# Performance work log

Hardware: AMD Instinct MI355X
Metric: run time of the kernel (lower is better)

Reference implementation:

```python
import jax, jax.numpy as jnp
import numpy as np

B, T, ENC_IN, DEC_IN, U = 32768, 7, 60, 36, 356


def setup_inputs() -> dict:
    key = jax.random.key(0)
    ks = jax.random.split(key, 12)
    s = 0.05  # small weight scale for numerical sanity
    return {
        "x_batch": jax.random.normal(ks[0], (B, T, ENC_IN), jnp.float32),
        "m_batch": jax.random.normal(ks[1], (B, T, DEC_IN), jnp.float32),
        "enc_kernel": jax.random.normal(ks[2], (ENC_IN, 4 * U), jnp.float32) * s,
        "enc_rec_kernel": jax.random.normal(ks[3], (U, 4 * U), jnp.float32) * s,
        "enc_bias": jnp.zeros((4 * U,), jnp.float32),
        "dec_kernel": jax.random.normal(ks[4], (DEC_IN, 4 * U), jnp.float32) * s,
        "dec_rec_kernel": jax.random.normal(ks[5], (U, 4 * U), jnp.float32) * s,
        "dec_bias": jnp.zeros((4 * U,), jnp.float32),
        "W_map": jax.random.normal(ks[6], (T * U, 768), jnp.float32) * s,
        "b_map": jnp.zeros((768,), jnp.float32),
        "W_deep1": jax.random.normal(ks[7], (768, 768), jnp.float32) * s,
        "b_deep1": jnp.zeros((768,), jnp.float32),
        "W_deep2": jax.random.normal(ks[8], (768, 768), jnp.float32) * s,
        "b_deep2": jnp.zeros((768,), jnp.float32),
        "W_out": jax.random.normal(ks[9], (768, 168), jnp.float32) * s,
        "b_out": jnp.zeros((168,), jnp.float32),
    }


def _lstm(x, K, R, b, h0, c0):
    """Keras-style LSTM. x: [B,T,D]. Returns (hs [B,T,U], h_T, c_T).
    Gate order i, f, g(candidate), o; sigmoid recurrent activation, tanh activation."""
    xz = jnp.einsum('btd,dg->btg', x, K) + b  # precompute input projections [B,T,4U]

    def step(carry, xz_t):
        h, c = carry
        z = xz_t + h @ R
        i, f, g, o = jnp.split(z, 4, axis=-1)
        c = jax.nn.sigmoid(f) * c + jax.nn.sigmoid(i) * jnp.tanh(g)
        h = jax.nn.sigmoid(o) * jnp.tanh(c)
        return (h, c), h

    (h, c), hs = jax.lax.scan(step, (h0, c0), jnp.swapaxes(xz, 0, 1))
    return jnp.swapaxes(hs, 0, 1), h, c


def reference(x_batch, m_batch, enc_kernel, enc_rec_kernel, enc_bias,
              dec_kernel, dec_rec_kernel, dec_bias,
              W_map, b_map, W_deep1, b_deep1, W_deep2, b_deep2, W_out, b_out):
    b = x_batch.shape[0]
    z = jnp.zeros((b, U), x_batch.dtype)
    # encoder: only final states used
    _, s_h, s_c = _lstm(x_batch, enc_kernel, enc_rec_kernel, enc_bias, z, z)
    # decoder: full sequence, initialized with encoder states
    decoded, _, _ = _lstm(m_batch, dec_kernel, dec_rec_kernel, dec_bias, s_h, s_c)
    f = decoded.reshape(b, -1)  # [B, 7*356]
    m = jax.nn.relu(f @ W_map + b_map)
    d = jnp.tanh(m @ W_deep1 + b_deep1)
    d = jnp.tanh(d @ W_deep2 + b_deep2)
    return d @ W_out + b_out
```

## Files before the change

### kernel.cpp

```cpp
#include <hip/hip_runtime.h>

typedef unsigned short u16;
typedef __attribute__((ext_vector_type(8))) short short8;
typedef __attribute__((ext_vector_type(4))) float f32x4;

#define B_ROWS 32768
#define T_STEPS 7
#define ENC_INd 60
#define DEC_INd 36
#define UNITS 356
#define KP_LSTM 448
#define H_OFF 64
#define HID 768
#define OUTN 168
#define OUTNP 256
#define KMAP 2688
#define HALF_E 44040192ull
#define WLSTM_E 688128

__device__ __forceinline__ u16 f2b(float f) {
  unsigned u = __builtin_bit_cast(unsigned, f);
  u += 0x7fffu + ((u >> 16) & 1u);
  return (u16)(u >> 16);
}
__device__ __forceinline__ float sigm(float x) { return 1.0f / (1.0f + __expf(-x)); }
__device__ __forceinline__ float tanhfast(float x) { return 2.0f / (1.0f + __expf(-2.0f * x)) - 1.0f; }

__global__ void fill_sentinel(float* __restrict__ out, int n, float v) {
  int i = blockIdx.x * 256 + threadIdx.x;
  int stride = gridDim.x * 256;
  for (; i < n; i += stride) out[i] = v;
}

__global__ void prep_lstm_w(const float* __restrict__ Km, const float* __restrict__ Rm,
                            const float* __restrict__ bias, int in_dim,
                            u16* __restrict__ WT, float* __restrict__ bias_r)
{
  int idx = blockIdx.x * 256 + threadIdx.x;
  if (idx >= WLSTM_E) return;
  int e    = idx & 7;
  int lane = (idx >> 3) & 63;
  int nf   = (idx >> 9) & 3;
  int t1   = idx >> 11;
  int kk   = t1 % 14;
  int g    = t1 / 14;
  int u = g * 16 + (lane & 15);
  int k = kk * 32 + ((lane >> 4) << 3) + e;
  float v = 0.f;
  if (u < UNITS) {
    int oc = nf * UNITS + u;
    if (k < in_dim) v = Km[(size_t)k * 1424 + oc];
    else if (k >= H_OFF && k < H_OFF + UNITS) v = Rm[(size_t)(k - H_OFF) * 1424 + oc];
    if (k == 0) bias_r[(u << 2) + nf] = bias[oc];
  } else if (k == 0) bias_r[(u << 2) + nf] = 0.f;
  WT[idx] = f2b(v);
}

__global__ void prep_map_w(const float* __restrict__ W, u16* __restrict__ WT)
{
  int idx = blockIdx.x * 256 + threadIdx.x;
  if (idx >= HID * KMAP) return;
  int n = idx / KMAP, k = idx - n * KMAP;
  int t = k / 384, kk = k - t * 384;
  float v = (kk < UNITS) ? W[(size_t)(t * UNITS + kk) * HID + n] : 0.f;
  WT[idx] = f2b(v);
}

__global__ void prep_mlp_w(const float* __restrict__ W, int korig, int norig, int kp,
                           u16* __restrict__ WT, int total)
{
  int idx = blockIdx.x * 256 + threadIdx.x;
  if (idx >= total) return;
  int n = idx / kp, k = idx - n * kp;
  float v = (k < korig && n < norig) ? W[(size_t)k * norig + n] : 0.f;
  WT[idx] = f2b(v);
}

__global__ __launch_bounds__(512)
void lstm_persistent(const float* __restrict__ xg, const float* __restrict__ mg,
                     const u16* __restrict__ WTe, const float* __restrict__ bre,
                     const u16* __restrict__ WTd, const float* __restrict__ brd,
                     u16* __restrict__ fbuf)
{
  __shared__ __align__(16) u16 A[2][32][KP_LSTM];

  const int tid = threadIdx.x;
  const int ns = tid >> 6;
  const int lane = tid & 63;
  const int l15 = lane & 15, l4 = lane >> 4;
  const int row0 = blockIdx.x * 32;

  float c_reg[3][2][4];
#pragma unroll
  for (int a = 0; a < 3; ++a)
#pragma unroll
    for (int b = 0; b < 2; ++b)
      c_reg[a][b][0] = c_reg[a][b][1] = c_reg[a][b][2] = c_reg[a][b][3] = 0.f;

  {
    short8 z = {};
    for (int q = tid; q < 2 * 32 * 48; q += 512) {
      int buf = q / 1536, rem = q - buf * 1536;
      int row = rem / 48, blk = 8 + (rem - row * 48);
      *(short8*)&A[buf][row][blk << 3] = z;
    }
  }

#pragma unroll 1
  for (int s = 0; s < 14; ++s) {
    const u16*  wt = (s < 7) ? WTe : WTd;
    const float* br = (s < 7) ? bre : brd;
    const float* src = (s < 7) ? xg : mg;
    const int in_dim = (s < 7) ? ENC_INd : DEC_INd;
    const int t = (s < 7) ? s : s - 7;
    const int par = s & 1;

    if (tid < 256) {
      const int row = tid >> 3, cb = tid & 7;
      const float* sp = src + ((size_t)(row0 + row) * T_STEPS + t) * in_dim;
      const int cbs = cb ^ (row & 7);
      short8 vv;
#pragma unroll
      for (int j = 0; j < 8; ++j) {
        const int cc = (cb << 3) + j;
        float v = (cc < in_dim) ? sp[cc] : 0.f;
        vv[j] = (short)f2b(v);
      }
      *(short8*)&A[par][row][cbs << 3] = vv;
    }
    __syncthreads();

#pragma unroll 1
    for (int p = 0; p < 3; ++p) {
      const int g = p * 8 + ns;
      f32x4 acc[2][4] = {};
      const u16* bp = wt + ((size_t)g * 14) * 2048 + (lane << 3);

#pragma unroll 2
      for (int kk = 0; kk < 14; ++kk) {
        short8 af[2], bf[4];
#pragma unroll
        for (int mf = 0; mf < 2; ++mf) {
          const int ra = (mf << 4) + l15;
          const int cbA = (kk << 2) + l4;
          const int cbs = (cbA & 56) | ((cbA ^ ra) & 7);
          af[mf] = *(const short8*)&A[par][ra][cbs << 3];
        }
#pragma unroll
        for (int nf = 0; nf < 4; ++nf)
          bf[nf] = *(const short8*)(bp + kk * 2048 + (nf << 9));
#pragma unroll
        for (int mf = 0; mf < 2; ++mf)
#pragma unroll
          for (int nf = 0; nf < 4; ++nf)
            acc[mf][nf] = __builtin_amdgcn_mfma_f32_16x16x32_bf16(af[mf], bf[nf], acc[mf][nf], 0, 0, 0);
      }

      const int u = (g << 4) + l15;
      const int ch = H_OFF + u, cbh = ch >> 3, cih = ch & 7;
      float bz[4];
#pragma unroll
      for (int nf = 0; nf < 4; ++nf) bz[nf] = br[(u << 2) + nf];
#pragma unroll
      for (int mf = 0; mf < 2; ++mf)
#pragma unroll
        for (int r = 0; r < 4; ++r) {
          const int row = (mf << 4) + (l4 << 2) + r;
          float zi = acc[mf][0][r] + bz[0];
          float zf = acc[mf][1][r] + bz[1];
          float zg = acc[mf][2][r] + bz[2];
          float zo = acc[mf][3][r] + bz[3];
          float ig = sigm(zi), fg = sigm(zf);
          float gg = tanhfast(zg), og = sigm(zo);
          float cn = fg * c_reg[p][mf][r] + ig * gg;
          c_reg[p][mf][r] = cn;
          float hv = og * tanhfast(cn);
          u16 hb = f2b(hv);
          const int cbs = (cbh & 56) | ((cbh ^ row) & 7);
          A[par ^ 1][row][(cbs << 3) + cih] = hb;
          if (s >= 7) {
            const int grow = row0 + row;
            fbuf[(size_t)(grow >> 14) * HALF_E
                 + ((size_t)(grow & 16383) * T_STEPS + t) * 384 + u] = hb;
          }
        }
    }
  }
}

template<int MODE>
__global__ __launch_bounds__(256)
void mlp_gemm(const u16* __restrict__ A, int lda, int kp,
              const u16* __restrict__ WT, const float* __restrict__ bias, int nreal,
              u16* __restrict__ outb, float* __restrict__ outf, int ldo)
{
  __shared__ __align__(16) u16 lds_a[128 * 64];
  __shared__ __align__(16) u16 lds_b[128 * 64];
  const int tid = threadIdx.x;
  const int wid = tid >> 6, lane = tid & 63;
  const int wm = (wid >> 1) << 6, wn = (wid & 1) << 6;
  const int l15 = lane & 15, l4 = lane >> 4;
  const int r0 = tid >> 3, c8 = tid & 7;
  const size_t abase = (size_t)blockIdx.x * 128 * lda;
  const size_t bbase = (size_t)blockIdx.y * 128 * kp;

  f32x4 acc[4][4] = {};

  for (int kt = 0; kt < kp; kt += 64) {
#pragma unroll
    for (int p = 0; p < 4; ++p) {
      int r = r0 + p * 32;
      short8 va = *(const short8*)(A + abase + (size_t)r * lda + kt + (c8 << 3));
      *(short8*)&lds_a[(r << 6) + ((c8 ^ (r & 7)) << 3)] = va;
      short8 vb = *(const short8*)(WT + bbase + (size_t)r * kp + kt + (c8 << 3));
      *(short8*)&lds_b[(r << 6) + ((c8 ^ (r & 7)) << 3)] = vb;
    }
    __syncthreads();
#pragma unroll
    for (int kk = 0; kk < 2; ++kk) {
      short8 af[4], bfr[4];
#pragma unroll
      for (int mf = 0; mf < 4; ++mf) {
        int ra = wm + (mf << 4) + l15;
        int cb = (kk << 2) + l4;
        af[mf] = *(const short8*)&lds_a[(ra << 6) + ((cb ^ (ra & 7)) << 3)];
      }
#pragma unroll
      for (int nf = 0; nf < 4; ++nf) {
        int rb = wn + (nf << 4) + l15;
        int cb = (kk << 2) + l4;
        bfr[nf] = *(const short8*)&lds_b[(rb << 6) + ((cb ^ (rb & 7)) << 3)];
      }
#pragma unroll
      for (int mf = 0; mf < 4; ++mf)
#pragma unroll
        for (int nf = 0; nf < 4; ++nf)
          acc[mf][nf] = __builtin_amdgcn_mfma_f32_16x16x32_bf16(af[mf], bfr[nf], acc[mf][nf], 0, 0, 0);
    }
    __syncthreads();
  }

#pragma unroll
  for (int mf = 0; mf < 4; ++mf) {
    int rowb = blockIdx.x * 128 + wm + (mf << 4) + (l4 << 2);
#pragma unroll
    for (int r = 0; r < 4; ++r) {
      int row = rowb + r;
#pragma unroll
      for (int nf = 0; nf < 4; ++nf) {
        int n = blockIdx.y * 128 + wn + (nf << 4) + l15;
        float v = acc[mf][nf][r];
        size_t oi = (size_t)row * ldo + n;
        if (MODE == 3) {
          outb[oi] = f2b(tanhfast(v + bias[n]));
        } else if (MODE == 5) {
          outb[oi] = f2b(fmaxf(v + bias[n], 0.f));
        } else {
          if (n < nreal) outf[oi] = v + bias[n];
        }
      }
    }
  }
}

extern "C" void kernel_launch(void* const* d_in, const int* in_sizes, int n_in,
                              void* d_out, int out_size, void* d_ws, size_t ws_size,
                              hipStream_t stream)
{
  const float* x    = (const float*)d_in[0];
  const float* m    = (const float*)d_in[1];
  const float* ek   = (const float*)d_in[2];
  const float* erk  = (const float*)d_in[3];
  const float* eb   = (const float*)d_in[4];
  const float* dk   = (const float*)d_in[5];
  const float* drk  = (const float*)d_in[6];
  const float* dbi  = (const float*)d_in[7];
  const float* wmap = (const float*)d_in[8];
  const float* bmap = (const float*)d_in[9];
  const float* wd1  = (const float*)d_in[10];
  const float* bd1  = (const float*)d_in[11];
  const float* wd2  = (const float*)d_in[12];
  const float* bd2  = (const float*)d_in[13];
  const float* wout = (const float*)d_in[14];
  const float* bout = (const float*)d_in[15];

  char* ws = (char*)d_ws;
  size_t off = 0;
  auto alloc = [&](size_t bytes) { char* p = ws + off; off += (bytes + 255) & ~(size_t)255; return p; };

  u16*   WT_enc  = (u16*)  alloc((size_t)WLSTM_E * 2);
  u16*   WT_dec  = (u16*)  alloc((size_t)WLSTM_E * 2);
  float* b_enc_r = (float*)alloc((size_t)384 * 4 * 4);
  float* b_dec_r = (float*)alloc((size_t)384 * 4 * 4);
  u16*   WT_map  = (u16*)  alloc((size_t)HID * KMAP * 2);
  u16*   WT_d1   = (u16*)  alloc((size_t)HID * HID * 2);
  u16*   WT_d2   = (u16*)  alloc((size_t)HID * HID * 2);
  u16*   WT_out  = (u16*)  alloc((size_t)OUTNP * HID * 2);
  u16*   m1_h1   = (u16*)  alloc((size_t)16384 * HID * 2);
  u16*   fbuf    = (u16*)  alloc((size_t)2 * HALF_E * 2);
  const size_t NEED = off;

  if (ws_size < NEED) {
    fill_sentinel<<<256, 256, 0, stream>>>((float*)d_out, out_size, (float)(ws_size >> 20));
    return;
  }

  u16* fb_h0 = fbuf;
  u16* fb_h1 = fbuf + HALF_E;
  u16* m1_h0 = fb_h1;
  u16* m2_h0 = fb_h0;
  u16* m2_h1 = fb_h0 + (size_t)16384 * HID;
  u16* m3_h0 = fb_h1;
  u16* m3_h1 = m1_h1;

  prep_lstm_w<<<(WLSTM_E + 255) / 256, 256, 0, stream>>>(ek, erk, eb, ENC_INd, WT_enc, b_enc_r);
  prep_lstm_w<<<(WLSTM_E + 255) / 256, 256, 0, stream>>>(dk, drk, dbi, DEC_INd, WT_dec, b_dec_r);
  prep_map_w<<<((HID * KMAP) + 255) / 256, 256, 0, stream>>>(wmap, WT_map);
  prep_mlp_w<<<((HID * HID) + 255) / 256, 256, 0, stream>>>(wd1, HID, HID, HID, WT_d1, HID * HID);
  prep_mlp_w<<<((HID * HID) + 255) / 256, 256, 0, stream>>>(wd2, HID, HID, HID, WT_d2, HID * HID);
  prep_mlp_w<<<((OUTNP * HID) + 255) / 256, 256, 0, stream>>>(wout, HID, OUTN, HID, WT_out, OUTNP * HID);

  lstm_persistent<<<1024, 512, 0, stream>>>(x, m, WT_enc, b_enc_r, WT_dec, b_dec_r, fbuf);

  mlp_gemm<5><<<dim3(128, 6), 256, 0, stream>>>(fb_h1, KMAP, KMAP, WT_map, bmap, HID, m1_h1, nullptr, HID);
  mlp_gemm<5><<<dim3(128, 6), 256, 0, stream>>>(fb_h0, KMAP, KMAP, WT_map, bmap, HID, m1_h0, nullptr, HID);
  mlp_gemm<3><<<dim3(128, 6), 256, 0, stream>>>(m1_h0, HID, HID, WT_d1, bd1, HID, m2_h0, nullptr, HID);
  mlp_gemm<3><<<dim3(128, 6), 256, 0, stream>>>(m1_h1, HID, HID, WT_d1, bd1, HID, m2_h1, nullptr, HID);
  mlp_gemm<3><<<dim3(128, 6), 256, 0, stream>>>(m2_h0, HID, HID, WT_d2, bd2, HID, m3_h0, nullptr, HID);
  mlp_gemm<3><<<dim3(128, 6), 256, 0, stream>>>(m2_h1, HID, HID, WT_d2, bd2, HID, m3_h1, nullptr, HID);
  mlp_gemm<4><<<dim3(128, 2), 256, 0, stream>>>(m3_h0, HID, HID, WT_out, bout, OUTN,
                                                nullptr, (float*)d_out, OUTN);
  mlp_gemm<4><<<dim3(128, 2), 256, 0, stream>>>(m3_h1, HID, HID, WT_out, bout, OUTN,
                                                nullptr, (float*)d_out + (size_t)16384 * OUTN, OUTN);
}
```

Before: 1.460 ms.

## Double LSTM rows per block and spill cell state to scratch global memory

The persistent LSTM kernel now handles 64 batch rows per block (512 blocks) instead of 32, so each weight fragment loaded from global memory feeds twice as many MFMAs. Doubling the accumulators would push register pressure too high, so the cell state no longer lives in registers. It is written to and read back from global scratch each step, reusing the output buffer, an m1 buffer and a new workspace slice. This cuts weight traffic and instruction overhead in exchange for extra global memory traffic for cell state, a larger LDS footprint and possibly lower occupancy.

```diff
diff --git a/kernel.cpp b/kernel.cpp
--- a/kernel.cpp
+++ b/kernel.cpp
@@ -17,6 +17,7 @@
 #define KMAP 2688
 #define HALF_E 44040192ull
 #define WLSTM_E 688128
+#define CG_BLK 6144
 
 __device__ __forceinline__ u16 f2b(float f) {
   unsigned u = __builtin_bit_cast(unsigned, f);
@@ -80,29 +81,29 @@
 void lstm_persistent(const float* __restrict__ xg, const float* __restrict__ mg,
                      const u16* __restrict__ WTe, const float* __restrict__ bre,
                      const u16* __restrict__ WTd, const float* __restrict__ brd,
-                     u16* __restrict__ fbuf)
-{
-  __shared__ __align__(16) u16 A[2][32][KP_LSTM];
+                     u16* __restrict__ fbuf,
+                     f32x4* __restrict__ cg0, f32x4* __restrict__ cg1, f32x4* __restrict__ cg2)
+{
+  __shared__ __align__(16) u16 A[2][64][KP_LSTM];
 
   const int tid = threadIdx.x;
   const int ns = tid >> 6;
   const int lane = tid & 63;
   const int l15 = lane & 15, l4 = lane >> 4;
-  const int row0 = blockIdx.x * 32;
-
-  float c_reg[3][2][4];
-#pragma unroll
-  for (int a = 0; a < 3; ++a)
-#pragma unroll
-    for (int b = 0; b < 2; ++b)
-      c_reg[a][b][0] = c_reg[a][b][1] = c_reg[a][b][2] = c_reg[a][b][3] = 0.f;
+  const int blk = blockIdx.x;
+  const int row0 = blk * 64;
+
+  f32x4* cgb;
+  if (blk < 224)      cgb = cg0 + (size_t)blk * CG_BLK;
+  else if (blk < 480) cgb = cg1 + (size_t)(blk - 224) * CG_BLK;
+  else                cgb = cg2 + (size_t)(blk - 480) * CG_BLK;
 
   {
     short8 z = {};
-    for (int q = tid; q < 2 * 32 * 48; q += 512) {
-      int buf = q / 1536, rem = q - buf * 1536;
-      int row = rem / 48, blk = 8 + (rem - row * 48);
-      *(short8*)&A[buf][row][blk << 3] = z;
+    for (int q = tid; q < 6144; q += 512) {
+      int buf = q / 3072, rem = q - buf * 3072;
+      int row = rem / 48, blkc = 8 + (rem - row * 48);
+      *(short8*)&A[buf][row][blkc << 3] = z;
     }
   }
 
@@ -115,7 +116,7 @@
     const int t = (s < 7) ? s : s - 7;
     const int par = s & 1;
 
-    if (tid < 256) {
+    {
       const int row = tid >> 3, cb = tid & 7;
       const float* sp = src + ((size_t)(row0 + row) * T_STEPS + t) * in_dim;
       const int cbs = cb ^ (row & 7);
@@ -133,27 +134,44 @@
 #pragma unroll 1
     for (int p = 0; p < 3; ++p) {
       const int g = p * 8 + ns;
-      f32x4 acc[2][4] = {};
+      f32x4 acc[4][4] = {};
       const u16* bp = wt + ((size_t)g * 14) * 2048 + (lane << 3);
 
-#pragma unroll 2
+#pragma unroll 1
       for (int kk = 0; kk < 14; ++kk) {
-        short8 af[2], bf[4];
-#pragma unroll
-        for (int mf = 0; mf < 2; ++mf) {
-          const int ra = (mf << 4) + l15;
-          const int cbA = (kk << 2) + l4;
-          const int cbs = (cbA & 56) | ((cbA ^ ra) & 7);
-          af[mf] = *(const short8*)&A[par][ra][cbs << 3];
-        }
+        short8 bf[4];
 #pragma unroll
         for (int nf = 0; nf < 4; ++nf)
           bf[nf] = *(const short8*)(bp + kk * 2048 + (nf << 9));
-#pragma unroll
-        for (int mf = 0; mf < 2; ++mf)
-#pragma unroll
-          for (int nf = 0; nf < 4; ++nf)
-            acc[mf][nf] = __builtin_amdgcn_mfma_f32_16x16x32_bf16(af[mf], bf[nf], acc[mf][nf], 0, 0, 0);
+        const int cbA = (kk << 2) + l4;
+        {
+          short8 af0[2];
+#pragma unroll
+          for (int mf = 0; mf < 2; ++mf) {
+            const int ra = (mf << 4) + l15;
+            const int cbs = (cbA & 56) | ((cbA ^ ra) & 7);
+            af0[mf] = *(const short8*)&A[par][ra][cbs << 3];
+          }
+#pragma unroll
+          for (int mf = 0; mf < 2; ++mf)
+#pragma unroll
+            for (int nf = 0; nf < 4; ++nf)
+              acc[mf][nf] = __builtin_amdgcn_mfma_f32_16x16x32_bf16(af0[mf], bf[nf], acc[mf][nf], 0, 0, 0);
+        }
+        {
+          short8 af1[2];
+#pragma unroll
+          for (int mf = 0; mf < 2; ++mf) {
+            const int ra = ((mf + 2) << 4) + l15;
+            const int cbs = (cbA & 56) | ((cbA ^ ra) & 7);
+            af1[mf] = *(const short8*)&A[par][ra][cbs << 3];
+          }
+#pragma unroll
+          for (int mf = 0; mf < 2; ++mf)
+#pragma unroll
+            for (int nf = 0; nf < 4; ++nf)
+              acc[mf + 2][nf] = __builtin_amdgcn_mfma_f32_16x16x32_bf16(af1[mf], bf[nf], acc[mf + 2][nf], 0, 0, 0);
+        }
       }
 
       const int u = (g << 4) + l15;
@@ -162,7 +180,11 @@
 #pragma unroll
       for (int nf = 0; nf < 4; ++nf) bz[nf] = br[(u << 2) + nf];
 #pragma unroll
-      for (int mf = 0; mf < 2; ++mf)
+      for (int mf = 0; mf < 4; ++mf) {
+        const int ci = (p * 4 + mf) * 512 + tid;
+        f32x4 cw;
+        if (s > 0) cw = cgb[ci];
+        else { cw[0] = 0.f; cw[1] = 0.f; cw[2] = 0.f; cw[3] = 0.f; }
 #pragma unroll
         for (int r = 0; r < 4; ++r) {
           const int row = (mf << 4) + (l4 << 2) + r;
@@ -172,8 +194,8 @@
           float zo = acc[mf][3][r] + bz[3];
           float ig = sigm(zi), fg = sigm(zf);
           float gg = tanhfast(zg), og = sigm(zo);
-          float cn = fg * c_reg[p][mf][r] + ig * gg;
-          c_reg[p][mf][r] = cn;
+          float cn = fg * cw[r] + ig * gg;
+          cw[r] = cn;
           float hv = og * tanhfast(cn);
           u16 hb = f2b(hv);
           const int cbs = (cbh & 56) | ((cbh ^ row) & 7);
@@ -184,6 +206,8 @@
                  + ((size_t)(grow & 16383) * T_STEPS + t) * 384 + u] = hb;
           }
         }
+        cgb[ci] = cw;
+      }
     }
   }
 }
@@ -298,12 +322,16 @@
   u16*   WT_out  = (u16*)  alloc((size_t)OUTNP * HID * 2);
   u16*   m1_h1   = (u16*)  alloc((size_t)16384 * HID * 2);
   u16*   fbuf    = (u16*)  alloc((size_t)2 * HALF_E * 2);
+  f32x4* cg2     = (f32x4*)alloc((size_t)32 * CG_BLK * 16);
   const size_t NEED = off;
 
   if (ws_size < NEED) {
     fill_sentinel<<<256, 256, 0, stream>>>((float*)d_out, out_size, (float)(ws_size >> 20));
     return;
   }
+
+  f32x4* cg0 = (f32x4*)d_out;
+  f32x4* cg1 = (f32x4*)m1_h1;
 
   u16* fb_h0 = fbuf;
   u16* fb_h1 = fbuf + HALF_E;
@@ -320,7 +348,8 @@
   prep_mlp_w<<<((HID * HID) + 255) / 256, 256, 0, stream>>>(wd2, HID, HID, HID, WT_d2, HID * HID);
   prep_mlp_w<<<((OUTNP * HID) + 255) / 256, 256, 0, stream>>>(wout, HID, OUTN, HID, WT_out, OUTNP * HID);
 
-  lstm_persistent<<<1024, 512, 0, stream>>>(x, m, WT_enc, b_enc_r, WT_dec, b_dec_r, fbuf);
+  lstm_persistent<<<512, 512, 0, stream>>>(x, m, WT_enc, b_enc_r, WT_dec, b_dec_r, fbuf,
+                                           cg0, cg1, cg2);
 
   mlp_gemm<5><<<dim3(128, 6), 256, 0, stream>>>(fb_h1, KMAP, KMAP, WT_map, bmap, HID, m1_h1, nullptr, HID);
   mlp_gemm<5><<<dim3(128, 6), 256, 0, stream>>>(fb_h0, KMAP, KMAP, WT_map, bmap, HID, m1_h0, nullptr, HID);
```

Result: slower. 1.495 ms (+2.4%).
